# Performance work log

Measured on AMD Instinct MI355X. Metric: run time of the kernel, lower is better.

Reference implementation:

```python
import jax, jax.numpy as jnp
import numpy as np

N_NODES = 50000
N_EDGES = 800000
D_IN = 128
D_OUT = 128


def setup_inputs() -> dict:
    key = jax.random.key(0)
    k1, k2, k3, k4, k5 = jax.random.split(key, 5)
    x = jax.random.normal(k1, (N_NODES, D_IN), dtype=jnp.float32)
    # fc weight, torch Linear convention: [out_dim, in_dim]
    W = jax.random.normal(k2, (D_OUT, D_IN), dtype=jnp.float32) * (1.0 / np.sqrt(D_IN))
    # attn_fc weight: [1, 2*out_dim], no bias
    a = jax.random.normal(k3, (1, 2 * D_OUT), dtype=jnp.float32) * (1.0 / np.sqrt(2 * D_OUT))
    src = jax.random.randint(k4, (N_EDGES,), 0, N_NODES)
    dst = jax.random.randint(k5, (N_EDGES,), 0, N_NODES)
    return {"x": x, "W": W, "a": a, "src": src, "dst": dst}


def reference(x, W, a, src, dst):
    # h = fc(x)
    h = x @ W.T  # [N, D_OUT]
    # attn_fc(cat([h_src, h_dst])) == h_src @ a[:D] + h_dst @ a[D:] (linear, no bias),
    # so precompute per-node scalars instead of materializing [E, 2*D_OUT].
    a_src = a[0, :D_OUT]
    a_dst = a[0, D_OUT:]
    s = h @ a_src  # [N]
    d = h @ a_dst  # [N]
    e = jax.nn.sigmoid(s[src] + d[dst])[:, None]  # [E, 1]
    msg = e * h[src]  # [E, D_OUT]  edge gather + weight
    # reduce: f[v] = sum over incoming edges of e * h_src
    f = jax.ops.segment_sum(msg, dst, num_segments=N_NODES)  # [N, D_OUT]
    return f
```

## Files before the change

### kernel.cpp

```cpp
#include <hip/hip_runtime.h>
#include <hip/hip_bf16.h>
#include <stdint.h>

#define NN 50000
#define NE 800000
#define DD 128
#define NBKT 782
#define BCH 2048
#define BGRID ((NE + BCH - 1) / BCH)
#define CAP 1280
#define SPILL_CAP 32768
#define GROWS 64
#define GGRID ((NN + GROWS - 1) / GROWS)

typedef __attribute__((ext_vector_type(8))) unsigned short ushort8;
typedef __attribute__((ext_vector_type(8))) short short8;
typedef __attribute__((ext_vector_type(4))) float f32x4;

__device__ inline uint16_t f2bf(float f) {
    uint32_t u = __float_as_uint(f);
    return (uint16_t)((u + 0x7fffu + ((u >> 16) & 1u)) >> 16);
}
__device__ inline float bf_lo(uint32_t u) { return __uint_as_float(u << 16); }
__device__ inline float bf_hi(uint32_t u) { return __uint_as_float(u & 0xffff0000u); }

__global__ __launch_bounds__(256) void wconv_k(const float* __restrict__ W,
                                               uint16_t* __restrict__ Wb,
                                               int* __restrict__ cntg) {
    int t = threadIdx.x;
    if (blockIdx.x == 0) {
        for (int k = t; k < NBKT + 4; k += 256) cntg[k] = 0;
    }
    int i = blockIdx.x * 256 + t;
    if (i < DD * DD) Wb[i] = f2bf(W[i]);
}

__global__ __launch_bounds__(256) void gemm_mfma_k(const float* __restrict__ x,
                                                   const uint16_t* __restrict__ Wb,
                                                   const float* __restrict__ a,
                                                   uint16_t* __restrict__ hb,
                                                   float* __restrict__ sArr,
                                                   float* __restrict__ dArr) {
    __shared__ __align__(16) uint16_t hs[GROWS][136];
    const int t = threadIdx.x, l = t & 63, wid = t >> 6;
    const int r0 = blockIdx.x * GROWS;
    const int lr = l & 15, lk = l >> 4;

    f32x4 acc[8];
    #pragma unroll
    for (int c = 0; c < 8; ++c) acc[c] = f32x4{0.f, 0.f, 0.f, 0.f};

    const int arow = r0 + wid * 16 + lr;
    const bool rok = arow < NN;
    const float* xp = x + (size_t)arow * DD + lk * 8;

    #pragma unroll
    for (int kc = 0; kc < 4; ++kc) {
        short8 af;
        if (rok) {
            float4 v0 = *(const float4*)(xp + kc * 32);
            float4 v1 = *(const float4*)(xp + kc * 32 + 4);
            af[0] = (short)f2bf(v0.x); af[1] = (short)f2bf(v0.y);
            af[2] = (short)f2bf(v0.z); af[3] = (short)f2bf(v0.w);
            af[4] = (short)f2bf(v1.x); af[5] = (short)f2bf(v1.y);
            af[6] = (short)f2bf(v1.z); af[7] = (short)f2bf(v1.w);
        } else {
            af = short8{0,0,0,0,0,0,0,0};
        }
        #pragma unroll
        for (int c = 0; c < 8; ++c) {
            int col = c * 16 + lr;
            short8 bf_ = *(const short8*)(Wb + (size_t)col * DD + kc * 32 + lk * 8);
            acc[c] = __builtin_amdgcn_mfma_f32_16x16x32_bf16(af, bf_, acc[c], 0, 0, 0);
        }
    }

    float avs[8], avd[8];
    #pragma unroll
    for (int c = 0; c < 8; ++c) {
        avs[c] = a[c * 16 + lr];
        avd[c] = a[DD + c * 16 + lr];
    }
    #pragma unroll
    for (int i = 0; i < 4; ++i) {
        float ps = 0.f, pd = 0.f;
        #pragma unroll
        for (int c = 0; c < 8; ++c) {
            ps = fmaf(acc[c][i], avs[c], ps);
            pd = fmaf(acc[c][i], avd[c], pd);
        }
        #pragma unroll
        for (int o = 8; o > 0; o >>= 1) {
            ps += __shfl_xor(ps, o);
            pd += __shfl_xor(pd, o);
        }
        if (lr == 0) {
            int row = r0 + wid * 16 + lk * 4 + i;
            if (row < NN) { sArr[row] = ps; dArr[row] = pd; }
        }
    }
    #pragma unroll
    for (int c = 0; c < 8; ++c)
        #pragma unroll
        for (int i = 0; i < 4; ++i)
            hs[wid * 16 + lk * 4 + i][c * 16 + lr] = f2bf(acc[c][i]);
    __syncthreads();

    {
        int row = t >> 2, cb = (t & 3) * 32;
        int grow = r0 + row;
        if (grow < NN) {
            #pragma unroll
            for (int k = 0; k < 4; ++k) {
                ushort8 v = *(const ushort8*)&hs[row][cb + k * 8];
                *(ushort8*)(hb + (size_t)grow * DD + cb + k * 8) = v;
            }
        }
    }
}

__global__ __launch_bounds__(256) void bscat_k(const int* __restrict__ src,
                                               const int* __restrict__ dst,
                                               int* __restrict__ cntg,
                                               int* __restrict__ spill_cnt,
                                               uint32_t* __restrict__ rec,
                                               uint2* __restrict__ spill) {
    __shared__ int lh[NBKT];
    __shared__ int gb[NBKT];
    int t = threadIdx.x;
    for (int k = t; k < NBKT; k += 256) lh[k] = 0;
    __syncthreads();
    int base = blockIdx.x * BCH;
    unsigned pk[8]; int bk[8];
    #pragma unroll
    for (int i = 0; i < 8; ++i) {
        int idx = base + i * 256 + t;
        if (idx < NE) {
            int s_ = src[idx], d_ = dst[idx];
            bk[i] = d_ >> 6;
            pk[i] = ((unsigned)(d_ & 63) << 16) | (unsigned)s_;
            atomicAdd(&lh[bk[i]], 1);
        } else bk[i] = -1;
    }
    __syncthreads();
    for (int k = t; k < NBKT; k += 256) {
        int c = lh[k];
        lh[k] = 0;
        if (c) gb[k] = atomicAdd(&cntg[k], c);
    }
    __syncthreads();
    #pragma unroll
    for (int i = 0; i < 8; ++i) {
        if (bk[i] >= 0) {
            int sl = atomicAdd(&lh[bk[i]], 1);
            int p = gb[bk[i]] + sl;
            if (p < CAP) {
                rec[(size_t)bk[i] * CAP + p] = pk[i];
            } else {
                int sp = atomicAdd(spill_cnt, 1);
                if (sp < SPILL_CAP)
                    spill[sp] = make_uint2(pk[i] & 0xffffu,
                                           (unsigned)(bk[i] * 64 + (int)(pk[i] >> 16)));
            }
        }
    }
}

__global__ __launch_bounds__(512) void bsort_agg_k(const uint32_t* __restrict__ hb,
                                                   const float* __restrict__ sA,
                                                   const float* __restrict__ dA,
                                                   const int* __restrict__ cntg,
                                                   const uint32_t* __restrict__ rec,
                                                   float* __restrict__ out) {
    __shared__ uint32_t srt[CAP];
    __shared__ float    eL[CAP];
    __shared__ float dAl[64];
    __shared__ int h64[64];
    __shared__ int s65[65];
    __shared__ int curw[64];
    int t = threadIdx.x, l = t & 63, wid = t >> 6;
    int b = blockIdx.x;
    int cnt = cntg[b]; if (cnt > CAP) cnt = CAP;
    int beg = b * CAP;
    int n0 = b * 64;
    if (t < 64) {
        h64[t] = 0;
        int n = n0 + t;
        dAl[t] = (n < NN) ? dA[n] : 0.f;
    }
    __syncthreads();

    uint32_t rc[3]; int nrc = 0;
    for (int j = t; j < cnt; j += 512) {
        uint32_t r = rec[beg + j];
        rc[nrc++] = r;
        atomicAdd(&h64[r >> 16], 1);
    }
    __syncthreads();
    if (wid == 0) {
        int v = h64[l];
        int inc = v;
        #pragma unroll
        for (int o = 1; o < 64; o <<= 1) {
            int nb = __shfl_up(inc, o);
            if (l >= o) inc += nb;
        }
        s65[l + 1] = inc;
        if (l == 0) s65[0] = 0;
        curw[l] = inc - v;
    }
    __syncthreads();
    for (int k = 0; k < nrc; ++k) {
        uint32_t r = rc[k];
        int d = (int)(r >> 16);
        int p = atomicAdd(&curw[d], 1);
        float z = sA[r & 0xffffu] + dAl[d];
        srt[p] = r;
        eL[p] = 1.f / (1.f + __expf(-z));
    }
    __syncthreads();
    #pragma unroll 1
    for (int rr = 0; rr < 8; ++rr) {
        int d = wid * 8 + rr;
        int n = n0 + d;
        if (n >= NN) break;
        int js = s65[d], je = s65[d + 1];
        float2 a0 = {0.f,0.f}, a1 = {0.f,0.f}, a2 = {0.f,0.f}, a3 = {0.f,0.f};
        int j = js;
        for (; j + 7 < je; j += 8) {
            uint32_t r0 = srt[j],   r1 = srt[j+1], r2 = srt[j+2], r3 = srt[j+3];
            uint32_t r4 = srt[j+4], r5 = srt[j+5], r6 = srt[j+6], r7 = srt[j+7];
            uint32_t u0 = hb[(size_t)(r0 & 0xffffu) * 64 + l];
            uint32_t u1 = hb[(size_t)(r1 & 0xffffu) * 64 + l];
            uint32_t u2 = hb[(size_t)(r2 & 0xffffu) * 64 + l];
            uint32_t u3 = hb[(size_t)(r3 & 0xffffu) * 64 + l];
            uint32_t u4 = hb[(size_t)(r4 & 0xffffu) * 64 + l];
            uint32_t u5 = hb[(size_t)(r5 & 0xffffu) * 64 + l];
            uint32_t u6 = hb[(size_t)(r6 & 0xffffu) * 64 + l];
            uint32_t u7 = hb[(size_t)(r7 & 0xffffu) * 64 + l];
            float e0 = eL[j],   e1 = eL[j+1], e2 = eL[j+2], e3 = eL[j+3];
            float e4 = eL[j+4], e5 = eL[j+5], e6 = eL[j+6], e7 = eL[j+7];
            a0.x = fmaf(e0, bf_lo(u0), a0.x); a0.y = fmaf(e0, bf_hi(u0), a0.y);
            a1.x = fmaf(e1, bf_lo(u1), a1.x); a1.y = fmaf(e1, bf_hi(u1), a1.y);
            a2.x = fmaf(e2, bf_lo(u2), a2.x); a2.y = fmaf(e2, bf_hi(u2), a2.y);
            a3.x = fmaf(e3, bf_lo(u3), a3.x); a3.y = fmaf(e3, bf_hi(u3), a3.y);
            a0.x = fmaf(e4, bf_lo(u4), a0.x); a0.y = fmaf(e4, bf_hi(u4), a0.y);
            a1.x = fmaf(e5, bf_lo(u5), a1.x); a1.y = fmaf(e5, bf_hi(u5), a1.y);
            a2.x = fmaf(e6, bf_lo(u6), a2.x); a2.y = fmaf(e6, bf_hi(u6), a2.y);
            a3.x = fmaf(e7, bf_lo(u7), a3.x); a3.y = fmaf(e7, bf_hi(u7), a3.y);
        }
        for (; j + 3 < je; j += 4) {
            uint32_t r0 = srt[j], r1 = srt[j+1], r2 = srt[j+2], r3 = srt[j+3];
            float e0 = eL[j], e1 = eL[j+1], e2 = eL[j+2], e3 = eL[j+3];
            uint32_t u0 = hb[(size_t)(r0 & 0xffffu) * 64 + l];
            uint32_t u1 = hb[(size_t)(r1 & 0xffffu) * 64 + l];
            uint32_t u2 = hb[(size_t)(r2 & 0xffffu) * 64 + l];
            uint32_t u3 = hb[(size_t)(r3 & 0xffffu) * 64 + l];
            a0.x = fmaf(e0, bf_lo(u0), a0.x); a0.y = fmaf(e0, bf_hi(u0), a0.y);
            a1.x = fmaf(e1, bf_lo(u1), a1.x); a1.y = fmaf(e1, bf_hi(u1), a1.y);
            a2.x = fmaf(e2, bf_lo(u2), a2.x); a2.y = fmaf(e2, bf_hi(u2), a2.y);
            a3.x = fmaf(e3, bf_lo(u3), a3.x); a3.y = fmaf(e3, bf_hi(u3), a3.y);
        }
        for (; j < je; ++j) {
            uint32_t r0 = srt[j];
            float e0 = eL[j];
            uint32_t u0 = hb[(size_t)(r0 & 0xffffu) * 64 + l];
            a0.x = fmaf(e0, bf_lo(u0), a0.x); a0.y = fmaf(e0, bf_hi(u0), a0.y);
        }
        float2 res;
        res.x = (a0.x + a1.x) + (a2.x + a3.x);
        res.y = (a0.y + a1.y) + (a2.y + a3.y);
        ((float2*)out)[(size_t)n * 64 + l] = res;
    }
}

__global__ __launch_bounds__(256) void spill_k(const int* __restrict__ spill_cnt,
                                               const uint2* __restrict__ spill,
                                               const float* __restrict__ sA,
                                               const float* __restrict__ dA,
                                               const uint32_t* __restrict__ hb,
                                               float* __restrict__ out) {
    int n = *spill_cnt; if (n > SPILL_CAP) n = SPILL_CAP;
    int w = blockIdx.x * 4 + (threadIdx.x >> 6), l = threadIdx.x & 63;
    for (int i = w; i < n; i += 32) {
        uint2 r = spill[i];
        float z = sA[r.x] + dA[r.y];
        float e = 1.f / (1.f + __expf(-z));
        uint32_t u = hb[(size_t)r.x * 64 + l];
        atomicAdd(&out[(size_t)r.y * DD + 2 * l],     e * bf_lo(u));
        atomicAdd(&out[(size_t)r.y * DD + 2 * l + 1], e * bf_hi(u));
    }
}

__global__ __launch_bounds__(256) void edge_atomic_k(const int* __restrict__ src, const int* __restrict__ dst,
                                                     const float* __restrict__ sArr, const float* __restrict__ dArr,
                                                     const uint32_t* __restrict__ hb, float* __restrict__ out) {
    int wid = threadIdx.x >> 6, l = threadIdx.x & 63;
    int e = blockIdx.x * 4 + wid;
    if (e >= NE) return;
    int sv = src[e], dv = dst[e];
    float z = sArr[sv] + dArr[dv];
    float ev = 1.0f / (1.0f + __expf(-z));
    uint32_t u = hb[(size_t)sv * 64 + l];
    atomicAdd(&out[(size_t)dv * DD + 2 * l],     ev * bf_lo(u));
    atomicAdd(&out[(size_t)dv * DD + 2 * l + 1], ev * bf_hi(u));
}

extern "C" void kernel_launch(void* const* d_in, const int* in_sizes, int n_in,
                              void* d_out, int out_size, void* d_ws, size_t ws_size,
                              hipStream_t stream) {
    const float* x  = (const float*)d_in[0];
    const float* W  = (const float*)d_in[1];
    const float* a  = (const float*)d_in[2];
    const int* src  = (const int*)d_in[3];
    const int* dst  = (const int*)d_in[4];
    float* out = (float*)d_out;

    char* p = (char*)d_ws;
    uint16_t* hb = (uint16_t*)p;            p += (size_t)NN * DD * 2;
    uint16_t* Wb = (uint16_t*)p;            p += (size_t)DD * DD * 2;
    float* sA    = (float*)p;               p += (size_t)NN * 4;
    float* dA    = (float*)p;               p += (size_t)NN * 4;
    int*   cntg  = (int*)p;                 p += (size_t)NBKT * 4;
    int*   scnt  = (int*)p;                 p += 16;
    uint32_t* rec = (uint32_t*)(((uintptr_t)p + 15) & ~(uintptr_t)15);
    p = (char*)(rec + (size_t)NBKT * CAP);
    uint2* spill = (uint2*)p;               p += (size_t)SPILL_CAP * 8;
    size_t need  = (size_t)(p - (char*)d_ws);

    if (ws_size >= need) {
        wconv_k<<<64, 256, 0, stream>>>(W, Wb, cntg);
        gemm_mfma_k<<<GGRID, 256, 0, stream>>>(x, Wb, a, hb, sA, dA);
        bscat_k<<<BGRID, 256, 0, stream>>>(src, dst, cntg, scnt, rec, spill);
        bsort_agg_k<<<NBKT, 512, 0, stream>>>((const uint32_t*)hb, sA, dA, cntg, rec, out);
        spill_k<<<8, 256, 0, stream>>>(scnt, spill, sA, dA, (const uint32_t*)hb, out);
    } else {
        hipMemsetAsync(out, 0, sizeof(float) * (size_t)NN * DD, stream);
        wconv_k<<<64, 256, 0, stream>>>(W, Wb, cntg);
        gemm_mfma_k<<<GGRID, 256, 0, stream>>>(x, Wb, a, hb, sA, dA);
        edge_atomic_k<<<NE / 4, 256, 0, stream>>>(src, dst, sA, dA, (const uint32_t*)hb, out);
    }
}
```

Before: 87.64 us.

## Fuse GEMM with edge bucketing, fold spill into aggregation, permute hb columns

Merges the MFMA projection kernel and the edge-bucket scatter kernel into a single launch, with blocks split by blockIdx, so the two independent stages overlap and one launch is dropped. The hb store now uses packed v_cvt_pk_bf16_f32 conversions written directly from registers in a permuted column order, removing the LDS staging and barrier. Output columns are un-permuted at the final store. The separate spill kernel is removed and spilled edges are handled inside the aggregation kernel by a linear scan, which could get costly if spills occur. The scatter chunk per block doubles, so fewer blocks do more work each.

```diff
diff --git a/kernel.cpp b/kernel.cpp
--- a/kernel.cpp
+++ b/kernel.cpp
@@ -6,7 +6,7 @@
 #define NE 800000
 #define DD 128
 #define NBKT 782
-#define BCH 2048
+#define BCH 4096
 #define BGRID ((NE + BCH - 1) / BCH)
 #define CAP 1280
 #define SPILL_CAP 32768
@@ -17,150 +17,143 @@
 typedef __attribute__((ext_vector_type(8))) short short8;
 typedef __attribute__((ext_vector_type(4))) float f32x4;
 
-__device__ inline uint16_t f2bf(float f) {
-    uint32_t u = __float_as_uint(f);
-    return (uint16_t)((u + 0x7fffu + ((u >> 16) & 1u)) >> 16);
+__device__ inline uint32_t cvtpk(float lo, float hi) {
+    uint32_t r;
+    asm("v_cvt_pk_bf16_f32 %0, %1, %2" : "=v"(r) : "v"(lo), "v"(hi));
+    return r;
 }
 __device__ inline float bf_lo(uint32_t u) { return __uint_as_float(u << 16); }
 __device__ inline float bf_hi(uint32_t u) { return __uint_as_float(u & 0xffff0000u); }
 
-__global__ __launch_bounds__(256) void wconv_k(const float* __restrict__ W,
-                                               uint16_t* __restrict__ Wb,
-                                               int* __restrict__ cntg) {
+__global__ __launch_bounds__(256) void prep_k(const float* __restrict__ W,
+                                              uint16_t* __restrict__ Wb,
+                                              int* __restrict__ cntg) {
     int t = threadIdx.x;
     if (blockIdx.x == 0) {
         for (int k = t; k < NBKT + 4; k += 256) cntg[k] = 0;
     }
     int i = blockIdx.x * 256 + t;
-    if (i < DD * DD) Wb[i] = f2bf(W[i]);
-}
-
-__global__ __launch_bounds__(256) void gemm_mfma_k(const float* __restrict__ x,
-                                                   const uint16_t* __restrict__ Wb,
-                                                   const float* __restrict__ a,
-                                                   uint16_t* __restrict__ hb,
-                                                   float* __restrict__ sArr,
-                                                   float* __restrict__ dArr) {
-    __shared__ __align__(16) uint16_t hs[GROWS][136];
-    const int t = threadIdx.x, l = t & 63, wid = t >> 6;
-    const int r0 = blockIdx.x * GROWS;
-    const int lr = l & 15, lk = l >> 4;
-
-    f32x4 acc[8];
-    #pragma unroll
-    for (int c = 0; c < 8; ++c) acc[c] = f32x4{0.f, 0.f, 0.f, 0.f};
-
-    const int arow = r0 + wid * 16 + lr;
-    const bool rok = arow < NN;
-    const float* xp = x + (size_t)arow * DD + lk * 8;
-
-    #pragma unroll
-    for (int kc = 0; kc < 4; ++kc) {
-        short8 af;
-        if (rok) {
-            float4 v0 = *(const float4*)(xp + kc * 32);
-            float4 v1 = *(const float4*)(xp + kc * 32 + 4);
-            af[0] = (short)f2bf(v0.x); af[1] = (short)f2bf(v0.y);
-            af[2] = (short)f2bf(v0.z); af[3] = (short)f2bf(v0.w);
-            af[4] = (short)f2bf(v1.x); af[5] = (short)f2bf(v1.y);
-            af[6] = (short)f2bf(v1.z); af[7] = (short)f2bf(v1.w);
-        } else {
-            af = short8{0,0,0,0,0,0,0,0};
-        }
-        #pragma unroll
-        for (int c = 0; c < 8; ++c) {
-            int col = c * 16 + lr;
-            short8 bf_ = *(const short8*)(Wb + (size_t)col * DD + kc * 32 + lk * 8);
-            acc[c] = __builtin_amdgcn_mfma_f32_16x16x32_bf16(af, bf_, acc[c], 0, 0, 0);
-        }
-    }
-
-    float avs[8], avd[8];
-    #pragma unroll
-    for (int c = 0; c < 8; ++c) {
-        avs[c] = a[c * 16 + lr];
-        avd[c] = a[DD + c * 16 + lr];
-    }
-    #pragma unroll
-    for (int i = 0; i < 4; ++i) {
-        float ps = 0.f, pd = 0.f;
-        #pragma unroll
-        for (int c = 0; c < 8; ++c) {
-            ps = fmaf(acc[c][i], avs[c], ps);
-            pd = fmaf(acc[c][i], avd[c], pd);
-        }
-        #pragma unroll
-        for (int o = 8; o > 0; o >>= 1) {
-            ps += __shfl_xor(ps, o);
-            pd += __shfl_xor(pd, o);
-        }
-        if (lr == 0) {
-            int row = r0 + wid * 16 + lk * 4 + i;
-            if (row < NN) { sArr[row] = ps; dArr[row] = pd; }
-        }
-    }
-    #pragma unroll
-    for (int c = 0; c < 8; ++c)
-        #pragma unroll
-        for (int i = 0; i < 4; ++i)
-            hs[wid * 16 + lk * 4 + i][c * 16 + lr] = f2bf(acc[c][i]);
-    __syncthreads();
-
-    {
-        int row = t >> 2, cb = (t & 3) * 32;
-        int grow = r0 + row;
-        if (grow < NN) {
-            #pragma unroll
-            for (int k = 0; k < 4; ++k) {
-                ushort8 v = *(const ushort8*)&hs[row][cb + k * 8];
-                *(ushort8*)(hb + (size_t)grow * DD + cb + k * 8) = v;
-            }
-        }
-    }
-}
-
-__global__ __launch_bounds__(256) void bscat_k(const int* __restrict__ src,
+    if (i < DD * DD) {
+        uint32_t u = __float_as_uint(W[i]);
+        Wb[i] = (uint16_t)((u + 0x7fffu + ((u >> 16) & 1u)) >> 16);
+    }
+}
+
+__global__ __launch_bounds__(256) void fused_k(const float* __restrict__ x,
+                                               const uint16_t* __restrict__ Wb,
+                                               const float* __restrict__ a,
+                                               const int* __restrict__ src,
                                                const int* __restrict__ dst,
+                                               uint16_t* __restrict__ hb,
+                                               float* __restrict__ sArr,
+                                               float* __restrict__ dArr,
                                                int* __restrict__ cntg,
-                                               int* __restrict__ spill_cnt,
+                                               int* __restrict__ scnt,
                                                uint32_t* __restrict__ rec,
                                                uint2* __restrict__ spill) {
     __shared__ int lh[NBKT];
     __shared__ int gb[NBKT];
-    int t = threadIdx.x;
-    for (int k = t; k < NBKT; k += 256) lh[k] = 0;
-    __syncthreads();
-    int base = blockIdx.x * BCH;
-    unsigned pk[8]; int bk[8];
-    #pragma unroll
-    for (int i = 0; i < 8; ++i) {
-        int idx = base + i * 256 + t;
-        if (idx < NE) {
-            int s_ = src[idx], d_ = dst[idx];
-            bk[i] = d_ >> 6;
-            pk[i] = ((unsigned)(d_ & 63) << 16) | (unsigned)s_;
-            atomicAdd(&lh[bk[i]], 1);
-        } else bk[i] = -1;
-    }
-    __syncthreads();
-    for (int k = t; k < NBKT; k += 256) {
-        int c = lh[k];
-        lh[k] = 0;
-        if (c) gb[k] = atomicAdd(&cntg[k], c);
-    }
-    __syncthreads();
-    #pragma unroll
-    for (int i = 0; i < 8; ++i) {
-        if (bk[i] >= 0) {
-            int sl = atomicAdd(&lh[bk[i]], 1);
-            int p = gb[bk[i]] + sl;
-            if (p < CAP) {
-                rec[(size_t)bk[i] * CAP + p] = pk[i];
-            } else {
-                int sp = atomicAdd(spill_cnt, 1);
-                if (sp < SPILL_CAP)
-                    spill[sp] = make_uint2(pk[i] & 0xffffu,
-                                           (unsigned)(bk[i] * 64 + (int)(pk[i] >> 16)));
+    const int t = threadIdx.x;
+
+    if ((int)blockIdx.x < GGRID) {
+        const int l = t & 63, wid = t >> 6;
+        const int r0 = blockIdx.x * GROWS;
+        const int lr = l & 15, lk = l >> 4;
+
+        f32x4 acc[8];
+        #pragma unroll
+        for (int c = 0; c < 8; ++c) acc[c] = f32x4{0.f, 0.f, 0.f, 0.f};
+
+        const int arow = r0 + wid * 16 + lr;
+        const int lrow = (arow < NN) ? arow : (NN - 1);
+        const float* xp = x + (size_t)lrow * DD + lk * 8;
+
+        #pragma unroll
+        for (int kc = 0; kc < 4; ++kc) {
+            float4 v0 = *(const float4*)(xp + kc * 32);
+            float4 v1 = *(const float4*)(xp + kc * 32 + 4);
+            union { uint32_t u[4]; short8 s; } A;
+            A.u[0] = cvtpk(v0.x, v0.y); A.u[1] = cvtpk(v0.z, v0.w);
+            A.u[2] = cvtpk(v1.x, v1.y); A.u[3] = cvtpk(v1.z, v1.w);
+            #pragma unroll
+            for (int c = 0; c < 8; ++c) {
+                int col = c * 16 + lr;
+                short8 bf_ = *(const short8*)(Wb + (size_t)col * DD + kc * 32 + lk * 8);
+                acc[c] = __builtin_amdgcn_mfma_f32_16x16x32_bf16(A.s, bf_, acc[c], 0, 0, 0);
+            }
+        }
+
+        float avs[8], avd[8];
+        #pragma unroll
+        for (int c = 0; c < 8; ++c) {
+            avs[c] = a[c * 16 + lr];
+            avd[c] = a[DD + c * 16 + lr];
+        }
+        #pragma unroll
+        for (int i = 0; i < 4; ++i) {
+            float ps = 0.f, pd = 0.f;
+            #pragma unroll
+            for (int c = 0; c < 8; ++c) {
+                ps = fmaf(acc[c][i], avs[c], ps);
+                pd = fmaf(acc[c][i], avd[c], pd);
+            }
+            #pragma unroll
+            for (int o = 8; o > 0; o >>= 1) {
+                ps += __shfl_xor(ps, o);
+                pd += __shfl_xor(pd, o);
+            }
+            int row = r0 + wid * 16 + lk * 4 + i;
+            if (lr == 0 && row < NN) { sArr[row] = ps; dArr[row] = pd; }
+        }
+
+        #pragma unroll
+        for (int i = 0; i < 4; ++i) {
+            int row = r0 + wid * 16 + lk * 4 + i;
+            if (row < NN) {
+                union { uint32_t u[4]; ushort8 s; } H;
+                H.u[0] = cvtpk(acc[0][i], acc[1][i]);
+                H.u[1] = cvtpk(acc[2][i], acc[3][i]);
+                H.u[2] = cvtpk(acc[4][i], acc[5][i]);
+                H.u[3] = cvtpk(acc[6][i], acc[7][i]);
+                *(ushort8*)(hb + (size_t)row * DD + lr * 8) = H.s;
+            }
+        }
+    } else {
+        int bb = blockIdx.x - GGRID;
+        for (int k = t; k < NBKT; k += 256) lh[k] = 0;
+        __syncthreads();
+        int base = bb * BCH;
+        unsigned pk[16]; int bk[16];
+        #pragma unroll
+        for (int i = 0; i < 16; ++i) {
+            int idx = base + i * 256 + t;
+            if (idx < NE) {
+                int s_ = src[idx], d_ = dst[idx];
+                bk[i] = d_ >> 6;
+                pk[i] = ((unsigned)(d_ & 63) << 16) | (unsigned)s_;
+                atomicAdd(&lh[bk[i]], 1);
+            } else bk[i] = -1;
+        }
+        __syncthreads();
+        for (int k = t; k < NBKT; k += 256) {
+            int c = lh[k];
+            lh[k] = 0;
+            if (c) gb[k] = atomicAdd(&cntg[k], c);
+        }
+        __syncthreads();
+        #pragma unroll
+        for (int i = 0; i < 16; ++i) {
+            if (bk[i] >= 0) {
+                int sl = atomicAdd(&lh[bk[i]], 1);
+                int p = gb[bk[i]] + sl;
+                if (p < CAP) {
+                    rec[(size_t)bk[i] * CAP + p] = pk[i];
+                } else {
+                    int sp = atomicAdd(scnt, 1);
+                    if (sp < SPILL_CAP)
+                        spill[sp] = make_uint2(pk[i] & 0xffffu,
+                                               (unsigned)(bk[i] * 64 + (int)(pk[i] >> 16)));
+                }
             }
         }
     }
@@ -171,6 +164,8 @@
                                                    const float* __restrict__ dA,
                                                    const int* __restrict__ cntg,
                                                    const uint32_t* __restrict__ rec,
+                                                   const int* __restrict__ scnt,
+                                                   const uint2* __restrict__ spill,
                                                    float* __restrict__ out) {
     __shared__ uint32_t srt[CAP];
     __shared__ float    eL[CAP];
@@ -183,6 +178,7 @@
     int cnt = cntg[b]; if (cnt > CAP) cnt = CAP;
     int beg = b * CAP;
     int n0 = b * 64;
+    int ns = *scnt; if (ns > SPILL_CAP) ns = SPILL_CAP;
     if (t < 64) {
         h64[t] = 0;
         int n = n0 + t;
@@ -219,6 +215,7 @@
         eL[p] = 1.f / (1.f + __expf(-z));
     }
     __syncthreads();
+    int colx = 32 * (l & 3) + (l >> 2);
     #pragma unroll 1
     for (int rr = 0; rr < 8; ++rr) {
         int d = wid * 8 + rr;
@@ -270,25 +267,21 @@
         float2 res;
         res.x = (a0.x + a1.x) + (a2.x + a3.x);
         res.y = (a0.y + a1.y) + (a2.y + a3.y);
-        ((float2*)out)[(size_t)n * 64 + l] = res;
-    }
-}
-
-__global__ __launch_bounds__(256) void spill_k(const int* __restrict__ spill_cnt,
-                                               const uint2* __restrict__ spill,
-                                               const float* __restrict__ sA,
-                                               const float* __restrict__ dA,
-                                               const uint32_t* __restrict__ hb,
-                                               float* __restrict__ out) {
-    int n = *spill_cnt; if (n > SPILL_CAP) n = SPILL_CAP;
-    int w = blockIdx.x * 4 + (threadIdx.x >> 6), l = threadIdx.x & 63;
-    for (int i = w; i < n; i += 32) {
-        uint2 r = spill[i];
-        float z = sA[r.x] + dA[r.y];
-        float e = 1.f / (1.f + __expf(-z));
-        uint32_t u = hb[(size_t)r.x * 64 + l];
-        atomicAdd(&out[(size_t)r.y * DD + 2 * l],     e * bf_lo(u));
-        atomicAdd(&out[(size_t)r.y * DD + 2 * l + 1], e * bf_hi(u));
+        if (ns > 0) {
+            for (int i = 0; i < ns; ++i) {
+                uint2 sp = spill[i];
+                if ((int)sp.y == n) {
+                    float z = sA[sp.x] + dAl[d];
+                    float e = 1.f / (1.f + __expf(-z));
+                    uint32_t u = hb[(size_t)sp.x * 64 + l];
+                    res.x = fmaf(e, bf_lo(u), res.x);
+                    res.y = fmaf(e, bf_hi(u), res.y);
+                }
+            }
+        }
+        float* orow = out + (size_t)n * DD;
+        orow[colx]      = res.x;
+        orow[colx + 16] = res.y;
     }
 }
 
@@ -302,8 +295,9 @@
     float z = sArr[sv] + dArr[dv];
     float ev = 1.0f / (1.0f + __expf(-z));
     uint32_t u = hb[(size_t)sv * 64 + l];
-    atomicAdd(&out[(size_t)dv * DD + 2 * l],     ev * bf_lo(u));
-    atomicAdd(&out[(size_t)dv * DD + 2 * l + 1], ev * bf_hi(u));
+    int colx = 32 * (l & 3) + (l >> 2);
+    atomicAdd(&out[(size_t)dv * DD + colx],      ev * bf_lo(u));
+    atomicAdd(&out[(size_t)dv * DD + colx + 16], ev * bf_hi(u));
 }
 
 extern "C" void kernel_launch(void* const* d_in, const int* in_sizes, int n_in,
@@ -329,15 +323,16 @@
     size_t need  = (size_t)(p - (char*)d_ws);
 
     if (ws_size >= need) {
-        wconv_k<<<64, 256, 0, stream>>>(W, Wb, cntg);
-        gemm_mfma_k<<<GGRID, 256, 0, stream>>>(x, Wb, a, hb, sA, dA);
-        bscat_k<<<BGRID, 256, 0, stream>>>(src, dst, cntg, scnt, rec, spill);
-        bsort_agg_k<<<NBKT, 512, 0, stream>>>((const uint32_t*)hb, sA, dA, cntg, rec, out);
-        spill_k<<<8, 256, 0, stream>>>(scnt, spill, sA, dA, (const uint32_t*)hb, out);
+        prep_k<<<64, 256, 0, stream>>>(W, Wb, cntg);
+        fused_k<<<GGRID + BGRID, 256, 0, stream>>>(x, Wb, a, src, dst,
+                                                   hb, sA, dA, cntg, scnt, rec, spill);
+        bsort_agg_k<<<NBKT, 512, 0, stream>>>((const uint32_t*)hb, sA, dA, cntg, rec,
+                                              scnt, spill, out);
     } else {
         hipMemsetAsync(out, 0, sizeof(float) * (size_t)NN * DD, stream);
-        wconv_k<<<64, 256, 0, stream>>>(W, Wb, cntg);
-        gemm_mfma_k<<<GGRID, 256, 0, stream>>>(x, Wb, a, hb, sA, dA);
+        prep_k<<<64, 256, 0, stream>>>(W, Wb, cntg);
+        fused_k<<<GGRID, 256, 0, stream>>>(x, Wb, a, src, dst,
+                                           hb, sA, dA, cntg, scnt, rec, spill);
         edge_atomic_k<<<NE / 4, 256, 0, stream>>>(src, dst, sA, dA, (const uint32_t*)hb, out);
     }
 }
```

Measured after the change: 72.63 us. 1.21x faster.
